# Kernel optimization log

Measured on AMD Instinct MI355X. Metric: run time of the kernel, lower is better.

## Reference

```python
import jax, jax.numpy as jnp
import numpy as np

N = 65536
INPUT_DIM = 4
HIDDEN = 256
OUT_DIM = 64
NUM_FREQS = 10
NUM_LAYERS = 4  # -> 3 residual blocks
NUM_COMPOSE = 4
DIN_PE = INPUT_DIM + 2 * INPUT_DIM * NUM_FREQS  # 84


def setup_inputs() -> dict:
    key = jax.random.key(0)
    ks = jax.random.split(key, 10)
    x = jax.random.uniform(ks[0], (N, INPUT_DIM), jnp.float32, 0.1, 1.0)
    in_dim = jax.random.uniform(ks[1], (N,), jnp.float32, 0.5, 1.5)
    layer_id = jax.random.randint(ks[2], (N,), 0, NUM_COMPOSE, dtype=jnp.int32)
    s0 = 1.0 / np.sqrt(DIN_PE)
    sh = 1.0 / np.sqrt(HIDDEN)
    W0 = jax.random.normal(ks[3], (NUM_COMPOSE, DIN_PE, HIDDEN), jnp.float32) * s0
    b0 = jax.random.normal(ks[4], (NUM_COMPOSE, HIDDEN), jnp.float32) * s0
    Wh = jax.random.normal(ks[5], (NUM_COMPOSE, NUM_LAYERS - 1, HIDDEN, HIDDEN), jnp.float32) * sh
    bh = jax.random.normal(ks[6], (NUM_COMPOSE, NUM_LAYERS - 1, HIDDEN), jnp.float32) * sh
    scal = jax.random.normal(ks[7], (NUM_COMPOSE, NUM_LAYERS - 1), jnp.float32) * 0.5
    Wout = jax.random.normal(ks[8], (NUM_COMPOSE, HIDDEN, OUT_DIM), jnp.float32) * sh
    bout = jax.random.normal(ks[9], (NUM_COMPOSE, OUT_DIM), jnp.float32) * sh
    return {"x": x, "in_dim": in_dim, "layer_id": layer_id, "W0": W0, "b0": b0,
            "Wh": Wh, "bh": bh, "scal": scal, "Wout": Wout, "bout": bout}


def _positional_encoding(x):
    # x: [N, D]; out order matches torch: [x, (sin,cos) for each freq i, each dim j]
    freqs = (2.0 ** jnp.arange(NUM_FREQS, dtype=x.dtype)) * np.pi  # [F]
    ang = x[:, None, :] * freqs[None, :, None]                      # [N, F, D]
    sc = jnp.stack([jnp.sin(ang), jnp.cos(ang)], axis=-1)           # [N, F, D, 2]
    return jnp.concatenate([x, sc.reshape(x.shape[0], -1)], axis=1)  # [N, D+2FD]


def reference(x, in_dim, layer_id, W0, b0, Wh, bh, scal, Wout, bout):
    # x[:, :3] = x[:, :3] / x[:, 3:]
    x = jnp.concatenate([x[:, :3] / x[:, 3:4], x[:, 3:]], axis=1)
    xe = _positional_encoding(x)  # [N, 84]

    def one_model(W0c, b0c, Whc, bhc, sc, Woutc, boutc):
        h = jax.nn.relu(xe @ W0c + b0c)           # [N, H]
        for k in range(NUM_LAYERS - 1):
            h = sc[k] * jax.nn.relu(h @ Whc[k] + bhc[k]) + h
        return h @ Woutc + boutc                  # [N, Dout]

    outs = jax.vmap(one_model)(W0, b0, Wh, bh, scal, Wout, bout)  # [C, N, Dout]
    # dispatch/combine: select each row's expert output
    out = jnp.take_along_axis(outs.transpose(1, 0, 2),
                              layer_id[:, None, None], axis=1)[:, 0]  # [N, Dout]
    return out / in_dim[:, None]
```

## Files before the change

### kernel.cpp

```cpp
#include <hip/hip_runtime.h>
#include <hip/hip_bf16.h>
#include <math.h>

#define N_ROWS 65536
#define H 256
#define DOUT 64
#define NC 4
#define NLAYERS_HIDDEN 3
#define DIN_PE 84
#define XE_STRIDE 104
#define BM 64
#define FB_STRIDE 68

#define CHUNK 512
#define WT0_PER_E 32768
#define WTH_PER_L 65536
#define WTOUT_PER_E 16384
#define N_WT0 (NC * WT0_PER_E)
#define N_WTH (NC * 3 * WTH_PER_L)
#define N_WTOUT (NC * WTOUT_PER_E)
#define N_PREP (N_WT0 + N_WTH + N_WTOUT)

using bf16 = __hip_bfloat16;
typedef __bf16 bf16x8 __attribute__((ext_vector_type(8)));
typedef float f32x4 __attribute__((ext_vector_type(4)));

__global__ void setup_kernel(const int* __restrict__ layer_id,
                             int* __restrict__ gcnt, int* __restrict__ idx,
                             const float* __restrict__ W0,
                             const float* __restrict__ Wh,
                             const float* __restrict__ Wout,
                             bf16* __restrict__ wt0, bf16* __restrict__ wth,
                             bf16* __restrict__ wtout) {
  const int bid = blockIdx.x;
  const int tid = threadIdx.x;
  if (bid < 256) {
    __shared__ int lcnt[NC];
    __shared__ int lbase[NC];
    if (tid < NC) lcnt[tid] = 0;
    __syncthreads();
    const int i = bid * 256 + tid;
    const int e = layer_id[i];
    const int lp = atomicAdd(&lcnt[e], 1);
    __syncthreads();
    if (tid < NC) lbase[tid] = atomicAdd(&gcnt[tid], lcnt[tid]);
    __syncthreads();
    idx[e * N_ROWS + lbase[e] + lp] = i;
    return;
  }
  const int i = (bid - 256) * 256 + tid;
  if (i < N_WT0) {
    int c = i >> 15, r = i & (WT0_PER_E - 1);
    int kbi = r >> 13, r2 = r & 8191;
    int nblk = r2 >> 9, w = r2 & 511;
    int lane = w >> 3, j = w & 7;
    int n = (nblk << 4) | (lane & 15);
    int k = (kbi << 5) | ((lane >> 4) << 3) | j;
    wt0[i] = __float2bfloat16(k < DIN_PE ? W0[(c * DIN_PE + k) * H + n] : 0.f);
  } else if (i < N_WT0 + N_WTH) {
    int u = i - N_WT0;
    int cl = u >> 16, r = u & 65535;
    int kbi = r >> 13;
    int nblk = (r >> 9) & 15, w = r & 511;
    int lane = w >> 3, j = w & 7;
    int n = (nblk << 4) | (lane & 15);
    int k = (kbi << 5) | ((lane >> 4) << 3) | j;
    wth[u] = __float2bfloat16(Wh[(cl << 16) | (k << 8) | n]);
  } else if (i < N_PREP) {
    int u = i - N_WT0 - N_WTH;
    int c = u >> 14, r = u & 16383;
    int kbi = r >> 11;
    int nblk = (r >> 9) & 3, w = r & 511;
    int lane = w >> 3, j = w & 7;
    int n = (nblk << 4) | (lane & 15);
    int k = (kbi << 5) | ((lane >> 4) << 3) | j;
    wtout[u] = __float2bfloat16(Wout[(c << 14) | (k << 6) | n]);
  }
}

__global__ __launch_bounds__(256, 3) void mlp_kernel(
    const float* __restrict__ x, const float* __restrict__ in_dim,
    const int* __restrict__ gcnt, const int* __restrict__ idx,
    const bf16* __restrict__ wt0, const float* __restrict__ b0,
    const bf16* __restrict__ wth, const float* __restrict__ bh,
    const float* __restrict__ scal, const bf16* __restrict__ wtout,
    const float* __restrict__ bout, float* __restrict__ out) {
  const int bid = blockIdx.x;
  const int c0 = gcnt[0], c1 = gcnt[1], c2 = gcnt[2], c3 = gcnt[3];
  const int n0 = (c0 + 63) >> 6, n1 = (c1 + 63) >> 6, n2 = (c2 + 63) >> 6,
            n3 = (c3 + 63) >> 6;
  int e, tb, cnt;
  if (bid < n0) { e = 0; tb = bid; cnt = c0; }
  else if (bid < n0 + n1) { e = 1; tb = bid - n0; cnt = c1; }
  else if (bid < n0 + n1 + n2) { e = 2; tb = bid - n0 - n1; cnt = c2; }
  else if (bid < n0 + n1 + n2 + n3) { e = 3; tb = bid - n0 - n1 - n2; cnt = c3; }
  else return;
  const int base = tb * BM;

  __shared__ int ridx[BM];
  __shared__ float indim_s[BM];
  __shared__ __align__(16) char smem[BM * H * 2];
  bf16* xe = (bf16*)smem;
  bf16* hs = (bf16*)smem;
  float* fbuf = (float*)smem;

  const int tid = threadIdx.x;
  if (tid < BM) {
    int p = base + tid;
    int ri = (p < cnt) ? idx[e * N_ROWS + p] : -1;
    ridx[tid] = ri;
    indim_s[tid] = (ri >= 0) ? in_dim[ri] : 1.f;
  }
  __syncthreads();

  {
    const int r = tid >> 2, d = tid & 3;
    const int ri = ridx[r];
    float xd = 0.f, x3 = 1.f;
    if (ri >= 0) { xd = x[ri * 4 + d]; x3 = x[ri * 4 + 3]; }
    float v = (d < 3) ? (xd / x3) : x3;
    if (ri < 0) v = 0.f;
    bf16* row = xe + r * XE_STRIDE;
    row[d] = __float2bfloat16(v);
    float f = 3.14159265358979323846f;
#pragma unroll 1
    for (int q = 0; q < 10; ++q) {
      float sn, cs;
      __sincosf(v * f, &sn, &cs);
      row[4 + q * 8 + d * 2] = __float2bfloat16(sn);
      row[4 + q * 8 + d * 2 + 1] = __float2bfloat16(cs);
      f *= 2.f;
    }
#pragma unroll 1
    for (int c = DIN_PE + d; c < XE_STRIDE; c += 4) row[c] = __float2bfloat16(0.f);
  }
  __syncthreads();

  const int lane = tid & 63;
  const int wid = tid >> 6;
  const int l15 = lane & 15;
  const int lq = lane >> 4;
  const int wb = wid * 64;

  f32x4 acc[4][4];

  {
    const bf16* W = wt0 + (size_t)e * WT0_PER_E + lane * 8;
    const float* bias = b0 + e * H + wb;
#pragma unroll
    for (int it = 0; it < 4; ++it) {
      f32x4 bv = *(const f32x4*)(bias + it * 16 + lq * 4);
#pragma unroll
      for (int jt = 0; jt < 4; ++jt) acc[it][jt] = bv;
    }
#pragma unroll 1
    for (int kb = 0; kb < 3; ++kb) {
      bf16x8 aw[4], bx[4];
#pragma unroll
      for (int it = 0; it < 4; ++it)
        aw[it] = *(const bf16x8*)(W + (kb * 16 + wid * 4 + it) * CHUNK);
#pragma unroll
      for (int jt = 0; jt < 4; ++jt)
        bx[jt] = *(const bf16x8*)(xe + (jt * 16 + l15) * XE_STRIDE + kb * 32 + lq * 8);
#pragma unroll
      for (int it = 0; it < 4; ++it)
#pragma unroll
        for (int jt = 0; jt < 4; ++jt)
          acc[it][jt] = __builtin_amdgcn_mfma_f32_16x16x32_bf16(
              aw[it], bx[jt], acc[it][jt], 0, 0, 0);
    }
    __syncthreads();
#pragma unroll
    for (int it = 0; it < 4; ++it)
#pragma unroll
      for (int jt = 0; jt < 4; ++jt) {
        int m = jt * 16 + l15;
        int nb = wb + it * 16 + lq * 4;
        int byte = ((m * H + nb) * 2) ^ ((l15 & 7) << 4);
        bf16 neu[4];
#pragma unroll
        for (int r = 0; r < 4; ++r)
          neu[r] = __float2bfloat16(fmaxf(acc[it][jt][r], 0.f));
        *(ushort4*)((char*)hs + byte) = *(ushort4*)neu;
      }
  }
  __syncthreads();

#pragma unroll 1
  for (int l = 0; l < NLAYERS_HIDDEN; ++l) {
    const bf16* W = wth + (size_t)(e * 3 + l) * WTH_PER_L + lane * 8;
    const float* bias = bh + (e * 3 + l) * H + wb;
    const float sc = scal[e * 3 + l];
#pragma unroll
    for (int it = 0; it < 4; ++it) {
      f32x4 bv = *(const f32x4*)(bias + it * 16 + lq * 4);
#pragma unroll
      for (int jt = 0; jt < 4; ++jt) acc[it][jt] = bv;
    }
    bf16x8 aw0[4], aw1[4];
#pragma unroll
    for (int it = 0; it < 4; ++it)
      aw0[it] = *(const bf16x8*)(W + (wid * 4 + it) * CHUNK);
#pragma unroll 1
    for (int kb = 0; kb < 8; kb += 2) {
#pragma unroll
      for (int it = 0; it < 4; ++it)
        aw1[it] = *(const bf16x8*)(W + ((kb + 1) * 16 + wid * 4 + it) * CHUNK);
      {
        bf16x8 bx[4];
#pragma unroll
        for (int jt = 0; jt < 4; ++jt) {
          int m = jt * 16 + l15;
          int byte = ((m * H + kb * 32 + lq * 8) * 2) ^ ((l15 & 7) << 4);
          bx[jt] = *(const bf16x8*)((const char*)hs + byte);
        }
#pragma unroll
        for (int it = 0; it < 4; ++it)
#pragma unroll
          for (int jt = 0; jt < 4; ++jt)
            acc[it][jt] = __builtin_amdgcn_mfma_f32_16x16x32_bf16(
                aw0[it], bx[jt], acc[it][jt], 0, 0, 0);
      }
      {
        int kn = (kb + 2) & 7;
#pragma unroll
        for (int it = 0; it < 4; ++it)
          aw0[it] = *(const bf16x8*)(W + (kn * 16 + wid * 4 + it) * CHUNK);
        bf16x8 bx[4];
#pragma unroll
        for (int jt = 0; jt < 4; ++jt) {
          int m = jt * 16 + l15;
          int byte = ((m * H + (kb + 1) * 32 + lq * 8) * 2) ^ ((l15 & 7) << 4);
          bx[jt] = *(const bf16x8*)((const char*)hs + byte);
        }
#pragma unroll
        for (int it = 0; it < 4; ++it)
#pragma unroll
          for (int jt = 0; jt < 4; ++jt)
            acc[it][jt] = __builtin_amdgcn_mfma_f32_16x16x32_bf16(
                aw1[it], bx[jt], acc[it][jt], 0, 0, 0);
      }
    }
    __syncthreads();
#pragma unroll
    for (int it = 0; it < 4; ++it)
#pragma unroll
      for (int jt = 0; jt < 4; ++jt) {
        int m = jt * 16 + l15;
        int nb = wb + it * 16 + lq * 4;
        int byte = ((m * H + nb) * 2) ^ ((l15 & 7) << 4);
        ushort4* p = (ushort4*)((char*)hs + byte);
        bf16 old[4]; *(ushort4*)old = *p;
        bf16 neu[4];
#pragma unroll
        for (int r = 0; r < 4; ++r) {
          float hv = sc * fmaxf(acc[it][jt][r], 0.f) + __bfloat162float(old[r]);
          neu[r] = __float2bfloat16(hv);
        }
        *p = *(ushort4*)neu;
      }
    __syncthreads();
  }

  {
    const bf16* W = wtout + (size_t)e * WTOUT_PER_E + lane * 8;
    const float* bias = bout + e * DOUT + wid * 16;
    f32x4 facc[4];
    f32x4 bv = *(const f32x4*)(bias + lq * 4);
#pragma unroll
    for (int jt = 0; jt < 4; ++jt) facc[jt] = bv;
    bf16x8 aw0, aw1;
    aw0 = *(const bf16x8*)(W + wid * CHUNK);
#pragma unroll 1
    for (int kb = 0; kb < 8; kb += 2) {
      aw1 = *(const bf16x8*)(W + ((kb + 1) * 4 + wid) * CHUNK);
      {
        bf16x8 bx[4];
#pragma unroll
        for (int jt = 0; jt < 4; ++jt) {
          int m = jt * 16 + l15;
          int byte = ((m * H + kb * 32 + lq * 8) * 2) ^ ((l15 & 7) << 4);
          bx[jt] = *(const bf16x8*)((const char*)hs + byte);
        }
#pragma unroll
        for (int jt = 0; jt < 4; ++jt)
          facc[jt] = __builtin_amdgcn_mfma_f32_16x16x32_bf16(aw0, bx[jt], facc[jt], 0, 0, 0);
      }
      {
        int kn = (kb + 2) & 7;
        aw0 = *(const bf16x8*)(W + (kn * 4 + wid) * CHUNK);
        bf16x8 bx[4];
#pragma unroll
        for (int jt = 0; jt < 4; ++jt) {
          int m = jt * 16 + l15;
          int byte = ((m * H + (kb + 1) * 32 + lq * 8) * 2) ^ ((l15 & 7) << 4);
          bx[jt] = *(const bf16x8*)((const char*)hs + byte);
        }
#pragma unroll
        for (int jt = 0; jt < 4; ++jt)
          facc[jt] = __builtin_amdgcn_mfma_f32_16x16x32_bf16(aw1, bx[jt], facc[jt], 0, 0, 0);
      }
    }
    __syncthreads();
#pragma unroll
    for (int jt = 0; jt < 4; ++jt) {
      int m = jt * 16 + l15;
      *(f32x4*)(fbuf + m * FB_STRIDE + wid * 16 + lq * 4) = facc[jt];
    }
  }
  __syncthreads();

#pragma unroll 1
  for (int p = 0; p < 4; ++p) {
    int item = p * 256 + tid;
    int row = item >> 4;
    int ch = item & 15;
    int ri = ridx[row];
    if (ri >= 0) {
      f32x4 v = *(const f32x4*)(fbuf + row * FB_STRIDE + ch * 4);
      float inv = indim_s[row];
      v[0] /= inv; v[1] /= inv; v[2] /= inv; v[3] /= inv;
      *(f32x4*)(out + (size_t)ri * DOUT + ch * 4) = v;
    }
  }
}

extern "C" void kernel_launch(void* const* d_in, const int* in_sizes, int n_in,
                              void* d_out, int out_size, void* d_ws,
                              size_t ws_size, hipStream_t stream) {
  const float* x = (const float*)d_in[0];
  const float* in_dim = (const float*)d_in[1];
  const int* layer_id = (const int*)d_in[2];
  const float* W0 = (const float*)d_in[3];
  const float* b0 = (const float*)d_in[4];
  const float* Wh = (const float*)d_in[5];
  const float* bh = (const float*)d_in[6];
  const float* scal = (const float*)d_in[7];
  const float* Wout = (const float*)d_in[8];
  const float* bout = (const float*)d_in[9];
  float* out = (float*)d_out;

  char* ws = (char*)d_ws;
  int* gcnt = (int*)ws;
  int* idx = (int*)(ws + 16);
  bf16* wt0 = (bf16*)(ws + 16 + (size_t)NC * N_ROWS * 4);
  bf16* wth = wt0 + N_WT0;
  bf16* wtout = wth + N_WTH;

  hipMemsetAsync(gcnt, 0, NC * sizeof(int), stream);
  setup_kernel<<<256 + N_PREP / 256, 256, 0, stream>>>(
      layer_id, gcnt, idx, W0, Wh, Wout, wt0, wth, wtout);
  mlp_kernel<<<N_ROWS / BM + NC - 1, 256, 0, stream>>>(
      x, in_dim, gcnt, idx, wt0, b0, wth, bh, scal, wtout, bout, out);
}
```

Baseline: 139.1 us.

## Triple-buffer weight fragments and prefetch next layer's weights across stages

Replaces the double-buffered per-layer weight loading with a fully unrolled three-deep register rotation. Each layer's first three k-blocks of weights are issued before the previous stage's epilogue and barrier, and the first-layer weights are fetched before the positional-encoding prologue. This is meant to hide global/L2 latency of weight loads behind MFMA work and barriers. It costs more live vector registers (12 extra bf16x8 fragments) under the launch bound of 3 blocks per SM, which risks spills.

Measured after the change: 182.8 us. 31.4% more time.

```diff
diff --git a/kernel.cpp b/kernel.cpp
--- a/kernel.cpp
+++ b/kernel.cpp
@@ -78,6 +78,37 @@
   }
 }
 
+#define HID_LOAD(AWP, KB)                                                  \
+  _Pragma("unroll") for (int it = 0; it < 4; ++it)                         \
+      AWP[it] = *(const bf16x8*)(W + ((KB) * 16 + wid * 4 + it) * CHUNK);
+
+#define HID_STEP(AWP, KB)                                                  \
+  {                                                                        \
+    bf16x8 bx[4];                                                          \
+    _Pragma("unroll") for (int jt = 0; jt < 4; ++jt) {                     \
+      int m = jt * 16 + l15;                                               \
+      int byte = ((m * H + (KB) * 32 + lq * 8) * 2) ^ ((l15 & 7) << 4);    \
+      bx[jt] = *(const bf16x8*)((const char*)hs + byte);                   \
+    }                                                                      \
+    _Pragma("unroll") for (int it = 0; it < 4; ++it)                       \
+        _Pragma("unroll") for (int jt = 0; jt < 4; ++jt)                   \
+            acc[it][jt] = __builtin_amdgcn_mfma_f32_16x16x32_bf16(         \
+                AWP[it], bx[jt], acc[it][jt], 0, 0, 0);                    \
+  }
+
+#define OUT_STEP(AWO, KB)                                                  \
+  {                                                                        \
+    bf16x8 bx[4];                                                          \
+    _Pragma("unroll") for (int jt = 0; jt < 4; ++jt) {                     \
+      int m = jt * 16 + l15;                                               \
+      int byte = ((m * H + (KB) * 32 + lq * 8) * 2) ^ ((l15 & 7) << 4);    \
+      bx[jt] = *(const bf16x8*)((const char*)hs + byte);                   \
+    }                                                                      \
+    _Pragma("unroll") for (int jt = 0; jt < 4; ++jt)                       \
+        facc[jt] = __builtin_amdgcn_mfma_f32_16x16x32_bf16(                \
+            AWO, bx[jt], facc[jt], 0, 0, 0);                               \
+  }
+
 __global__ __launch_bounds__(256, 3) void mlp_kernel(
     const float* __restrict__ x, const float* __restrict__ in_dim,
     const int* __restrict__ gcnt, const int* __restrict__ idx,
@@ -97,6 +128,22 @@
   else return;
   const int base = tb * BM;
 
+  const int tid = threadIdx.x;
+  const int lane = tid & 63;
+  const int wid = tid >> 6;
+  const int l15 = lane & 15;
+  const int lq = lane >> 4;
+  const int wb = wid * 64;
+
+  bf16x8 awp0[4], awp1[4], awp2[4];
+
+  {
+    const bf16* W = wt0 + (size_t)e * WT0_PER_E + lane * 8;
+    HID_LOAD(awp0, 0)
+    HID_LOAD(awp1, 1)
+    HID_LOAD(awp2, 2)
+  }
+
   __shared__ int ridx[BM];
   __shared__ float indim_s[BM];
   __shared__ __align__(16) char smem[BM * H * 2];
@@ -104,7 +151,6 @@
   bf16* hs = (bf16*)smem;
   float* fbuf = (float*)smem;
 
-  const int tid = threadIdx.x;
   if (tid < BM) {
     int p = base + tid;
     int ri = (p < cnt) ? idx[e * N_ROWS + p] : -1;
@@ -136,16 +182,9 @@
   }
   __syncthreads();
 
-  const int lane = tid & 63;
-  const int wid = tid >> 6;
-  const int l15 = lane & 15;
-  const int lq = lane >> 4;
-  const int wb = wid * 64;
-
   f32x4 acc[4][4];
 
   {
-    const bf16* W = wt0 + (size_t)e * WT0_PER_E + lane * 8;
     const float* bias = b0 + e * H + wb;
 #pragma unroll
     for (int it = 0; it < 4; ++it) {
@@ -153,21 +192,25 @@
 #pragma unroll
       for (int jt = 0; jt < 4; ++jt) acc[it][jt] = bv;
     }
-#pragma unroll 1
+#pragma unroll
     for (int kb = 0; kb < 3; ++kb) {
-      bf16x8 aw[4], bx[4];
-#pragma unroll
-      for (int it = 0; it < 4; ++it)
-        aw[it] = *(const bf16x8*)(W + (kb * 16 + wid * 4 + it) * CHUNK);
+      bf16x8 bx[4];
 #pragma unroll
       for (int jt = 0; jt < 4; ++jt)
         bx[jt] = *(const bf16x8*)(xe + (jt * 16 + l15) * XE_STRIDE + kb * 32 + lq * 8);
+      const bf16x8* awc = (kb == 0) ? awp0 : (kb == 1) ? awp1 : awp2;
 #pragma unroll
       for (int it = 0; it < 4; ++it)
 #pragma unroll
         for (int jt = 0; jt < 4; ++jt)
           acc[it][jt] = __builtin_amdgcn_mfma_f32_16x16x32_bf16(
-              aw[it], bx[jt], acc[it][jt], 0, 0, 0);
+              awc[it], bx[jt], acc[it][jt], 0, 0, 0);
+    }
+    {
+      const bf16* W = wth + (size_t)(e * 3) * WTH_PER_L + lane * 8;
+      HID_LOAD(awp0, 0)
+      HID_LOAD(awp1, 1)
+      HID_LOAD(awp2, 2)
     }
     __syncthreads();
 #pragma unroll
@@ -186,6 +229,8 @@
   }
   __syncthreads();
 
+  bf16x8 awo0, awo1, awo2;
+
 #pragma unroll 1
   for (int l = 0; l < NLAYERS_HIDDEN; ++l) {
     const bf16* W = wth + (size_t)(e * 3 + l) * WTH_PER_L + lane * 8;
@@ -197,49 +242,27 @@
 #pragma unroll
       for (int jt = 0; jt < 4; ++jt) acc[it][jt] = bv;
     }
-    bf16x8 aw0[4], aw1[4];
-#pragma unroll
-    for (int it = 0; it < 4; ++it)
-      aw0[it] = *(const bf16x8*)(W + (wid * 4 + it) * CHUNK);
-#pragma unroll 1
-    for (int kb = 0; kb < 8; kb += 2) {
-#pragma unroll
-      for (int it = 0; it < 4; ++it)
-        aw1[it] = *(const bf16x8*)(W + ((kb + 1) * 16 + wid * 4 + it) * CHUNK);
+    HID_STEP(awp0, 0) HID_LOAD(awp0, 3)
+    HID_STEP(awp1, 1) HID_LOAD(awp1, 4)
+    HID_STEP(awp2, 2) HID_LOAD(awp2, 5)
+    HID_STEP(awp0, 3) HID_LOAD(awp0, 6)
+    HID_STEP(awp1, 4) HID_LOAD(awp1, 7)
+    HID_STEP(awp2, 5)
+    HID_STEP(awp0, 6)
+    HID_STEP(awp1, 7)
+    if (l < NLAYERS_HIDDEN - 1) {
+      const bf16* W2 = wth + (size_t)(e * 3 + l + 1) * WTH_PER_L + lane * 8;
       {
-        bf16x8 bx[4];
-#pragma unroll
-        for (int jt = 0; jt < 4; ++jt) {
-          int m = jt * 16 + l15;
-          int byte = ((m * H + kb * 32 + lq * 8) * 2) ^ ((l15 & 7) << 4);
-          bx[jt] = *(const bf16x8*)((const char*)hs + byte);
-        }
-#pragma unroll
-        for (int it = 0; it < 4; ++it)
-#pragma unroll
-          for (int jt = 0; jt < 4; ++jt)
-            acc[it][jt] = __builtin_amdgcn_mfma_f32_16x16x32_bf16(
-                aw0[it], bx[jt], acc[it][jt], 0, 0, 0);
+        const bf16* W = W2;
+        HID_LOAD(awp0, 0)
+        HID_LOAD(awp1, 1)
+        HID_LOAD(awp2, 2)
       }
-      {
-        int kn = (kb + 2) & 7;
-#pragma unroll
-        for (int it = 0; it < 4; ++it)
-          aw0[it] = *(const bf16x8*)(W + (kn * 16 + wid * 4 + it) * CHUNK);
-        bf16x8 bx[4];
-#pragma unroll
-        for (int jt = 0; jt < 4; ++jt) {
-          int m = jt * 16 + l15;
-          int byte = ((m * H + (kb + 1) * 32 + lq * 8) * 2) ^ ((l15 & 7) << 4);
-          bx[jt] = *(const bf16x8*)((const char*)hs + byte);
-        }
-#pragma unroll
-        for (int it = 0; it < 4; ++it)
-#pragma unroll
-          for (int jt = 0; jt < 4; ++jt)
-            acc[it][jt] = __builtin_amdgcn_mfma_f32_16x16x32_bf16(
-                aw1[it], bx[jt], acc[it][jt], 0, 0, 0);
-      }
+    } else {
+      const bf16* Wo = wtout + (size_t)e * WTOUT_PER_E + lane * 8;
+      awo0 = *(const bf16x8*)(Wo + (0 * 4 + wid) * CHUNK);
+      awo1 = *(const bf16x8*)(Wo + (1 * 4 + wid) * CHUNK);
+      awo2 = *(const bf16x8*)(Wo + (2 * 4 + wid) * CHUNK);
     }
     __syncthreads();
 #pragma unroll
@@ -263,44 +286,20 @@
   }
 
   {
-    const bf16* W = wtout + (size_t)e * WTOUT_PER_E + lane * 8;
+    const bf16* Wo = wtout + (size_t)e * WTOUT_PER_E + lane * 8;
     const float* bias = bout + e * DOUT + wid * 16;
     f32x4 facc[4];
     f32x4 bv = *(const f32x4*)(bias + lq * 4);
 #pragma unroll
     for (int jt = 0; jt < 4; ++jt) facc[jt] = bv;
-    bf16x8 aw0, aw1;
-    aw0 = *(const bf16x8*)(W + wid * CHUNK);
-#pragma unroll 1
-    for (int kb = 0; kb < 8; kb += 2) {
-      aw1 = *(const bf16x8*)(W + ((kb + 1) * 4 + wid) * CHUNK);
-      {
-        bf16x8 bx[4];
-#pragma unroll
-        for (int jt = 0; jt < 4; ++jt) {
-          int m = jt * 16 + l15;
-          int byte = ((m * H + kb * 32 + lq * 8) * 2) ^ ((l15 & 7) << 4);
-          bx[jt] = *(const bf16x8*)((const char*)hs + byte);
-        }
-#pragma unroll
-        for (int jt = 0; jt < 4; ++jt)
-          facc[jt] = __builtin_amdgcn_mfma_f32_16x16x32_bf16(aw0, bx[jt], facc[jt], 0, 0, 0);
-      }
-      {
-        int kn = (kb + 2) & 7;
-        aw0 = *(const bf16x8*)(W + (kn * 4 + wid) * CHUNK);
-        bf16x8 bx[4];
-#pragma unroll
-        for (int jt = 0; jt < 4; ++jt) {
-          int m = jt * 16 + l15;
-          int byte = ((m * H + (kb + 1) * 32 + lq * 8) * 2) ^ ((l15 & 7) << 4);
-          bx[jt] = *(const bf16x8*)((const char*)hs + byte);
-        }
-#pragma unroll
-        for (int jt = 0; jt < 4; ++jt)
-          facc[jt] = __builtin_amdgcn_mfma_f32_16x16x32_bf16(aw1, bx[jt], facc[jt], 0, 0, 0);
-      }
-    }
+    OUT_STEP(awo0, 0) awo0 = *(const bf16x8*)(Wo + (3 * 4 + wid) * CHUNK);
+    OUT_STEP(awo1, 1) awo1 = *(const bf16x8*)(Wo + (4 * 4 + wid) * CHUNK);
+    OUT_STEP(awo2, 2) awo2 = *(const bf16x8*)(Wo + (5 * 4 + wid) * CHUNK);
+    OUT_STEP(awo0, 3) awo0 = *(const bf16x8*)(Wo + (6 * 4 + wid) * CHUNK);
+    OUT_STEP(awo1, 4) awo1 = *(const bf16x8*)(Wo + (7 * 4 + wid) * CHUNK);
+    OUT_STEP(awo2, 5)
+    OUT_STEP(awo0, 6)
+    OUT_STEP(awo1, 7)
     __syncthreads();
 #pragma unroll
     for (int jt = 0; jt < 4; ++jt) {
```
